# Kernel tuning notes

Measured on AMD Instinct MI355X. Metric: run time of the kernel, lower is better.

The kernel has to match this reference:

```python
import jax, jax.numpy as jnp
import numpy as np

NUM_HEADS = 32
NUM_KV_HEADS = 8
HEAD_DIM = 128
ROPE_THETA = 10000.0


def _rope_cos_sin(seq_len, head_dim, dtype):
    inv_freq = 1.0 / (ROPE_THETA ** (jnp.arange(0, head_dim, 2, dtype=jnp.float32) / head_dim))
    t = jnp.arange(seq_len, dtype=jnp.float32)
    freqs = jnp.outer(t, inv_freq)              # [S, hd/2]
    emb = jnp.concatenate([freqs, freqs], axis=-1)  # [S, hd]
    return jnp.cos(emb).astype(dtype), jnp.sin(emb).astype(dtype)


def _rotate_half(x):
    h = x.shape[-1] // 2
    return jnp.concatenate([-x[..., h:], x[..., :h]], axis=-1)


def _apply_rope(x, cos, sin):
    # x: [B, H, S, D]; cos/sin: [S, D] (position_ids = arange(S) in prefill)
    return x * cos[None, None] + _rotate_half(x) * sin[None, None]


def setup_inputs() -> dict:
    key = jax.random.key(0)
    ks = jax.random.split(key, 5)
    B, S, H = 1, 2048, 4096
    return {
        "hidden_states": jax.random.normal(ks[0], (B, S, H), dtype=jnp.float32),
        "Wq": jax.random.normal(ks[1], (H, NUM_HEADS * HEAD_DIM), dtype=jnp.float32) * 0.02,
        "Wk": jax.random.normal(ks[2], (H, NUM_KV_HEADS * HEAD_DIM), dtype=jnp.float32) * 0.02,
        "Wv": jax.random.normal(ks[3], (H, NUM_KV_HEADS * HEAD_DIM), dtype=jnp.float32) * 0.02,
        "Wo": jax.random.normal(ks[4], (NUM_HEADS * HEAD_DIM, H), dtype=jnp.float32) * 0.02,
    }


def reference(hidden_states, Wq, Wk, Wv, Wo):
    B, S, H = hidden_states.shape
    nh, nkv, hd = NUM_HEADS, NUM_KV_HEADS, HEAD_DIM
    groups = nh // nkv

    # fused QKV projections (bias-free, Llama-style)
    q = (hidden_states @ Wq).reshape(B, S, nh, hd).transpose(0, 2, 1, 3)   # [B,nh,S,D]
    k = (hidden_states @ Wk).reshape(B, S, nkv, hd).transpose(0, 2, 1, 3)  # [B,nkv,S,D]
    v = (hidden_states @ Wv).reshape(B, S, nkv, hd).transpose(0, 2, 1, 3)

    # inline RoPE on q and k
    cos, sin = _rope_cos_sin(S, hd, q.dtype)
    q = _apply_rope(q, cos, sin)
    k = _apply_rope(k, cos, sin)

    # GQA: repeat kv heads to match query heads (num_key_value_groups)
    k = jnp.repeat(k, groups, axis=1)  # [B,nh,S,D]
    v = jnp.repeat(v, groups, axis=1)

    scale = 1.0 / jnp.sqrt(jnp.asarray(hd, dtype=q.dtype))
    logits = jnp.einsum("bhqd,bhkd->bhqk", q, k) * scale  # [B,nh,S,S]

    # prefill causal mask (phys_past_len = 0)
    causal = jnp.tril(jnp.ones((S, S), dtype=bool))
    neg = jnp.asarray(jnp.finfo(logits.dtype).min, dtype=logits.dtype)
    logits = jnp.where(causal[None, None], logits, neg)

    attn = jax.nn.softmax(logits.astype(jnp.float32), axis=-1).astype(q.dtype)
    out = jnp.einsum("bhqk,bhkd->bhqd", attn, v)           # [B,nh,S,D]
    out = out.transpose(0, 2, 1, 3).reshape(B, S, nh * hd)  # [B,S,H]
    return out @ Wo
```

## Files before the change

### kernel.cpp

```cpp
#include <hip/hip_runtime.h>
#include <cstdint>
#include <cstddef>

typedef __attribute__((ext_vector_type(4))) float f32x4;
typedef __attribute__((ext_vector_type(16))) float f32x16;
typedef __attribute__((ext_vector_type(8))) short bf16x8;
typedef __attribute__((ext_vector_type(2))) unsigned int u32x2;

#define S_LEN   2048
#define HID     4096
#define NH      32
#define NKV     8
#define HD      128
#define QKV_N   6144

typedef const __attribute__((address_space(1))) unsigned int* gptr_t;
typedef __attribute__((address_space(3))) unsigned int* lptr_t;

__device__ __forceinline__ void gload_lds16(const void* g, void* l) {
  __builtin_amdgcn_global_load_lds((gptr_t)g, (lptr_t)l, 16, 0, 0);
}

__device__ __forceinline__ ushort f2bf(float f) {
  union { float f; uint32_t u; } v; v.f = f;
  uint32_t r = v.u + 0x7FFFu + ((v.u >> 16) & 1u);
  return (ushort)(r >> 16);
}
__device__ __forceinline__ float bf2f(ushort u) {
  union { uint32_t u; float f; } v; v.u = ((uint32_t)u) << 16;
  return v.f;
}

__global__ void cast_f32_bf16(const float* __restrict__ in, ushort* __restrict__ out, int n) {
  int i = (blockIdx.x * 256 + threadIdx.x) * 4;
  if (i >= n) return;
  float4 v = *reinterpret_cast<const float4*>(in + i);
  ushort4 o;
  o.x = f2bf(v.x); o.y = f2bf(v.y); o.z = f2bf(v.z); o.w = f2bf(v.w);
  *reinterpret_cast<ushort4*>(out + i) = o;
}

__global__ void transpose_cast(const float* __restrict__ in, ushort* __restrict__ out, int R, int C) {
  __shared__ float t[32][33];
  int tx = threadIdx.x & 31, ty = threadIdx.x >> 5;
  int r0 = blockIdx.y * 32, c0 = blockIdx.x * 32;
#pragma unroll
  for (int i = 0; i < 32; i += 8)
    t[ty + i][tx] = in[(size_t)(r0 + ty + i) * C + c0 + tx];
  __syncthreads();
#pragma unroll
  for (int i = 0; i < 32; i += 8)
    out[(size_t)(c0 + ty + i) * R + r0 + tx] = f2bf(t[tx][ty + i]);
}

template <bool BF16_OUT>
__global__ __launch_bounds__(256, 4) void gemm_bt(
    const ushort* __restrict__ A, const ushort* __restrict__ B,
    void* __restrict__ Cp, int M, int N, int K) {
  __shared__ ushort a_lds[128 * 32];
  __shared__ ushort b_lds[128 * 32];
  const int tid = threadIdx.x;
  const int wid = tid >> 6, lane = tid & 63;
  const int l16 = lane & 15, lk = lane >> 4;
  const int wr = wid >> 1, wc = wid & 1;
  const size_t a_row0 = (size_t)blockIdx.y * 128;
  const size_t b_row0 = (size_t)blockIdx.x * 128;

  f32x4 acc[4][4] = {};
  const int pswz = lk ^ (l16 & 3) ^ ((l16 >> 2) & 1);

  for (int kt = 0; kt < K; kt += 32) {
    __syncthreads();
#pragma unroll
    for (int i = 0; i < 2; ++i) {
      int c = i * 256 + tid;
      int row = c >> 2, p = c & 3;
      int gch = p ^ (row & 3) ^ ((row >> 2) & 1);
      gload_lds16(A + (a_row0 + row) * K + kt + gch * 8, &a_lds[c * 8]);
      gload_lds16(B + (b_row0 + row) * K + kt + gch * 8, &b_lds[c * 8]);
    }
    __syncthreads();

    bf16x8 af[4], bf[4];
#pragma unroll
    for (int m = 0; m < 4; ++m) {
      int row = wr * 64 + m * 16 + l16;
      af[m] = *reinterpret_cast<const bf16x8*>(&a_lds[row * 32 + pswz * 8]);
    }
#pragma unroll
    for (int n = 0; n < 4; ++n) {
      int row = wc * 64 + n * 16 + l16;
      bf[n] = *reinterpret_cast<const bf16x8*>(&b_lds[row * 32 + pswz * 8]);
    }
#pragma unroll
    for (int m = 0; m < 4; ++m)
#pragma unroll
      for (int n = 0; n < 4; ++n)
        acc[m][n] = __builtin_amdgcn_mfma_f32_16x16x32_bf16(af[m], bf[n], acc[m][n], 0, 0, 0);
  }

#pragma unroll
  for (int m = 0; m < 4; ++m) {
    int row_b = wr * 64 + m * 16 + lk * 4;
#pragma unroll
    for (int n = 0; n < 4; ++n) {
      int col = (int)b_row0 + wc * 64 + n * 16 + l16;
#pragma unroll
      for (int r = 0; r < 4; ++r) {
        size_t row = a_row0 + row_b + r;
        if constexpr (BF16_OUT)
          ((ushort*)Cp)[row * N + col] = f2bf(acc[m][n][r]);
        else
          ((float*)Cp)[row * N + col] = acc[m][n][r];
      }
    }
  }
}

__global__ void rope_kernel(ushort* __restrict__ QKV) {
  int idx = blockIdx.x * 256 + threadIdx.x;
  int dg = idx & 7;
  int t = idx >> 3;
  int s = t / 40;
  int hh = t - s * 40;
  if (s >= S_LEN) return;
  int col = (hh < NH) ? hh * HD : HID + (hh - NH) * HD;
  ushort* base = QKV + (size_t)s * QKV_N + col + dg * 8;

  union U { uint4 v; ushort u[8]; };
  U L, H, OL, OH;
  L.v = *reinterpret_cast<const uint4*>(base);
  H.v = *reinterpret_cast<const uint4*>(base + 64);
  const float C0 = 13.287712379549449f / 64.0f;
#pragma unroll
  for (int j = 0; j < 8; ++j) {
    int d = dg * 8 + j;
    float invf = exp2f(-(float)d * C0);
    float ang = (float)s * invf;
    float sn, cs;
    sincosf(ang, &sn, &cs);
    float xl = bf2f(L.u[j]), xh = bf2f(H.u[j]);
    OL.u[j] = f2bf(xl * cs - xh * sn);
    OH.u[j] = f2bf(xh * cs + xl * sn);
  }
  *reinterpret_cast<uint4*>(base) = OL.v;
  *reinterpret_cast<uint4*>(base + 64) = OH.v;
}

__global__ void transpose_v(const ushort* __restrict__ QKV, ushort* __restrict__ Vt) {
  __shared__ ushort t[64][65];
  int s0 = blockIdx.x * 64;
  int d0 = blockIdx.y * 64;
  int hkv = blockIdx.z;
  int tx = threadIdx.x & 63, ty = threadIdx.x >> 6;
#pragma unroll
  for (int i = 0; i < 64; i += 4)
    t[i + ty][tx] = QKV[(size_t)(s0 + i + ty) * QKV_N + HID + NKV * HD + hkv * HD + d0 + tx];
  __syncthreads();
#pragma unroll
  for (int i = 0; i < 64; i += 4)
    Vt[((size_t)hkv * HD + d0 + i + ty) * S_LEN + s0 + tx] = t[tx][i + ty];
}

__global__ __launch_bounds__(256, 2) void attn_kernel(
    const ushort* __restrict__ QKV, const ushort* __restrict__ Vt, ushort* __restrict__ AO) {
  constexpr float SCALE = 0.08838834764831845f;
  __shared__ ushort k_lds[2][64 * 128];
  __shared__ ushort v_lds[2][128 * 64];

  const int lin = blockIdx.x;
  const int h = ((lin & 7) << 2) + ((lin >> 3) & 3);
  const int p = lin >> 5;
  const int hkv = h >> 2;
  const int tid = threadIdx.x, wid = tid >> 6, lane = tid & 63;
  const int l32 = lane & 31;
  const int hi = lane >> 5;

  auto stageKV = [&](int buf, int kt) {
#pragma unroll
    for (int i = 0; i < 4; ++i) {
      int c = i * 256 + wid * 64 + lane;
      int row = c >> 4, ch = c & 15;
      int sch = ch ^ (row & 7);
      gload_lds16(QKV + (size_t)(kt * 64 + row) * QKV_N + HID + hkv * HD + sch * 8,
                  &k_lds[buf][c * 8]);
    }
#pragma unroll
    for (int i = 0; i < 4; ++i) {
      int c = i * 256 + wid * 64 + lane;
      int row = c >> 3, ch = c & 7;
      int sch = ch ^ (row & 7);
      gload_lds16(Vt + ((size_t)hkv * HD + row) * S_LEN + (size_t)kt * 64 + sch * 8,
                  &v_lds[buf][c * 8]);
    }
  };

  for (int pi = 0; pi < 2; ++pi) {
    const int qb = pi ? (15 - p) : p;
    const int q0 = qb * 128;
    const int qg = q0 + wid * 32 + l32;

    bf16x8 qf[8];
    {
      const ushort* qrow = QKV + (size_t)qg * QKV_N + h * HD + hi * 8;
#pragma unroll
      for (int ds = 0; ds < 8; ++ds)
        qf[ds] = *reinterpret_cast<const bf16x8*>(qrow + ds * 16);
    }

    float m_run = -1e30f, l_run = 0.f;
    f32x16 oacc[4] = {};

    stageKV(0, 0);
    __syncthreads();

    const int nt = 2 * qb + 2;
    for (int kt = 0; kt < nt; ++kt) {
      const int cur = kt & 1;
      if (kt + 1 < nt) stageKV(cur ^ 1, kt + 1);

      if (kt * 64 <= q0 + wid * 32 + 31) {
        float pv[32];
        __builtin_amdgcn_s_setprio(1);
#pragma unroll
        for (int kf = 0; kf < 2; ++kf) {
          f32x16 s = {};
          int rk = kf * 32 + l32;
#pragma unroll
          for (int ds = 0; ds < 8; ++ds) {
            int c16 = (ds * 2 + hi) ^ (rk & 7);
            bf16x8 kfr = *reinterpret_cast<const bf16x8*>(&k_lds[cur][rk * 128 + c16 * 8]);
            s = __builtin_amdgcn_mfma_f32_32x32x16_bf16(kfr, qf[ds], s, 0, 0, 0);
          }
#pragma unroll
          for (int r = 0; r < 16; ++r) pv[kf * 16 + r] = s[r] * SCALE;
        }
        __builtin_amdgcn_s_setprio(0);

        if (kt * 64 + 63 > q0 + wid * 32) {
#pragma unroll
          for (int kf = 0; kf < 2; ++kf)
#pragma unroll
            for (int r = 0; r < 16; ++r) {
              int kl = kf * 32 + (r & 3) + 8 * (r >> 2) + 4 * hi;
              if (kt * 64 + kl > qg) pv[kf * 16 + r] = -1e30f;
            }
        }

        float mt = pv[0];
#pragma unroll
        for (int i = 1; i < 32; ++i) mt = fmaxf(mt, pv[i]);
        mt = fmaxf(mt, __shfl_xor(mt, 32, 64));
        float mn = fmaxf(m_run, mt);
        float alpha = __expf(m_run - mn);
        float ls = 0.f;
#pragma unroll
        for (int i = 0; i < 32; ++i) { pv[i] = __expf(pv[i] - mn); ls += pv[i]; }
        ls += __shfl_xor(ls, 32, 64);
        l_run = l_run * alpha + ls;
        m_run = mn;
#pragma unroll
        for (int f = 0; f < 4; ++f)
#pragma unroll
          for (int r = 0; r < 16; ++r) oacc[f][r] *= alpha;

        union PW { uint32_t w[4]; bf16x8 v; } pa[4];
#pragma unroll
        for (int ks = 0; ks < 4; ++ks) {
          uint32_t x0, x1, y0, y1;
          asm("v_cvt_pk_bf16_f32 %0, %1, %2" : "=v"(x0) : "v"(pv[8 * ks + 0]), "v"(pv[8 * ks + 1]));
          asm("v_cvt_pk_bf16_f32 %0, %1, %2" : "=v"(x1) : "v"(pv[8 * ks + 2]), "v"(pv[8 * ks + 3]));
          asm("v_cvt_pk_bf16_f32 %0, %1, %2" : "=v"(y0) : "v"(pv[8 * ks + 4]), "v"(pv[8 * ks + 5]));
          asm("v_cvt_pk_bf16_f32 %0, %1, %2" : "=v"(y1) : "v"(pv[8 * ks + 6]), "v"(pv[8 * ks + 7]));
          u32x2 r0 = __builtin_amdgcn_permlane32_swap(x0, y0, false, false);
          u32x2 r1 = __builtin_amdgcn_permlane32_swap(x1, y1, false, false);
          pa[ks].w[0] = r0.x; pa[ks].w[1] = r1.x; pa[ks].w[2] = r0.y; pa[ks].w[3] = r1.y;
        }

        __builtin_amdgcn_s_setprio(1);
#pragma unroll
        for (int ks = 0; ks < 4; ++ks) {
#pragma unroll
          for (int f = 0; f < 4; ++f) {
            int dv = f * 32 + l32;
            int c8 = (2 * ks + hi) ^ (dv & 7);
            bf16x8 vfr = *reinterpret_cast<const bf16x8*>(&v_lds[cur][dv * 64 + c8 * 8]);
            oacc[f] = __builtin_amdgcn_mfma_f32_32x32x16_bf16(vfr, pa[ks].v, oacc[f], 0, 0, 0);
          }
        }
        __builtin_amdgcn_s_setprio(0);
      }

      __syncthreads();
    }

    float inv_l = 1.0f / l_run;
    ushort* aorow = AO + (size_t)qg * HID + h * HD;
#pragma unroll
    for (int f = 0; f < 4; ++f)
#pragma unroll
      for (int g = 0; g < 4; ++g) {
        ushort4 o;
        o.x = f2bf(oacc[f][g * 4 + 0] * inv_l);
        o.y = f2bf(oacc[f][g * 4 + 1] * inv_l);
        o.z = f2bf(oacc[f][g * 4 + 2] * inv_l);
        o.w = f2bf(oacc[f][g * 4 + 3] * inv_l);
        *reinterpret_cast<ushort4*>(aorow + f * 32 + g * 8 + 4 * hi) = o;
      }
  }
}

extern "C" void kernel_launch(void* const* d_in, const int* in_sizes, int n_in,
                              void* d_out, int out_size, void* d_ws, size_t ws_size,
                              hipStream_t stream) {
  (void)in_sizes; (void)n_in; (void)out_size;
  const float* hs = (const float*)d_in[0];
  const float* Wq = (const float*)d_in[1];
  const float* Wk = (const float*)d_in[2];
  const float* Wv = (const float*)d_in[3];
  const float* Wo = (const float*)d_in[4];
  float* out = (float*)d_out;

  char* ws = (char*)d_ws;
  const size_t OFF_HSB   = 0;
  const size_t OFF_WQKVT = OFF_HSB + 16777216;
  const size_t OFF_WOT   = OFF_WQKVT + 50331648;
  const size_t OFF_QKV   = OFF_WOT + 33554432;
  const size_t OFF_VT    = OFF_QKV + 25165824;
  const size_t OFF_AO    = OFF_VT + 4194304;
  if (ws_size < OFF_AO + 16777216) return;

  ushort* hsb   = (ushort*)(ws + OFF_HSB);
  ushort* WqkvT = (ushort*)(ws + OFF_WQKVT);
  ushort* WoT   = (ushort*)(ws + OFF_WOT);
  ushort* QKV   = (ushort*)(ws + OFF_QKV);
  ushort* Vt    = (ushort*)(ws + OFF_VT);
  ushort* AO    = (ushort*)(ws + OFF_AO);

  cast_f32_bf16<<<8192, 256, 0, stream>>>(hs, hsb, S_LEN * HID);
  transpose_cast<<<dim3(4096 / 32, 4096 / 32), 256, 0, stream>>>(Wq, WqkvT, HID, 4096);
  transpose_cast<<<dim3(1024 / 32, 4096 / 32), 256, 0, stream>>>(Wk, WqkvT + (size_t)4096 * HID, HID, 1024);
  transpose_cast<<<dim3(1024 / 32, 4096 / 32), 256, 0, stream>>>(Wv, WqkvT + (size_t)5120 * HID, HID, 1024);
  transpose_cast<<<dim3(4096 / 32, 4096 / 32), 256, 0, stream>>>(Wo, WoT, 4096, HID);

  gemm_bt<true><<<dim3(QKV_N / 128, S_LEN / 128), 256, 0, stream>>>(hsb, WqkvT, QKV, S_LEN, QKV_N, HID);
  rope_kernel<<<(S_LEN * 40 * 8) / 256, 256, 0, stream>>>(QKV);
  transpose_v<<<dim3(S_LEN / 64, HD / 64, NKV), 256, 0, stream>>>(QKV, Vt);
  attn_kernel<<<256, 256, 0, stream>>>(QKV, Vt, AO);
  gemm_bt<false><<<dim3(HID / 128, S_LEN / 128), 256, 0, stream>>>(AO, WoT, out, S_LEN, HID, HID);
}
```

Before: 355.1 us.

## Replace GEMM with triple-buffered pipelined 128x256 tile kernel using 8 waves

Swaps the single-buffered 128x128 GEMM for a 512-thread kernel with 128x256 tiles and a three-slot LDS ring. Global-to-LDS loads for k-tile t+2 are issued while computing tile t, synchronised with explicit vmcnt waits and raw barriers. The B fragment reads are split into two halves interleaved with MFMA bursts under raised wave priority, and the LDS swizzle pattern changes. The aim is to hide global load latency and raise MFMA utilisation in the QKV and output projections, at the cost of more LDS per block and fragile hand-tuned waitcnt counts.

```diff
diff --git a/kernel.cpp b/kernel.cpp
--- a/kernel.cpp
+++ b/kernel.cpp
@@ -53,65 +53,114 @@
     out[(size_t)(c0 + ty + i) * R + r0 + tx] = f2bf(t[tx][ty + i]);
 }
 
-template <bool BF16_OUT>
-__global__ __launch_bounds__(256, 4) void gemm_bt(
+template <int BM, bool BF16_OUT>
+__global__ __launch_bounds__(512, 2) void gemm_pipe(
     const ushort* __restrict__ A, const ushort* __restrict__ B,
-    void* __restrict__ Cp, int M, int N, int K) {
-  __shared__ ushort a_lds[128 * 32];
-  __shared__ ushort b_lds[128 * 32];
+    void* __restrict__ Cp, int N, int K) {
+  constexpr int MR = BM / 32;
+  constexpr int ALOADS = BM / 128;
+  __shared__ ushort a_lds[3][BM * 32];
+  __shared__ ushort b_lds[3][256 * 32];
   const int tid = threadIdx.x;
   const int wid = tid >> 6, lane = tid & 63;
   const int l16 = lane & 15, lk = lane >> 4;
-  const int wr = wid >> 1, wc = wid & 1;
-  const size_t a_row0 = (size_t)blockIdx.y * 128;
-  const size_t b_row0 = (size_t)blockIdx.x * 128;
-
-  f32x4 acc[4][4] = {};
-  const int pswz = lk ^ (l16 & 3) ^ ((l16 >> 2) & 1);
-
-  for (int kt = 0; kt < K; kt += 32) {
-    __syncthreads();
+  const int wr = wid >> 2, wc = wid & 3;
+  const size_t a_row0 = (size_t)blockIdx.y * BM;
+  const size_t b_row0 = (size_t)blockIdx.x * 256;
+
+  f32x4 acc[MR][4] = {};
+  const int NT = K >> 5;
+  const int cswz = lk ^ ((l16 >> 1) & 3);
+
+  auto stageA = [&](int slot, int t) {
+    const size_t kb = (size_t)t << 5;
+#pragma unroll
+    for (int i = 0; i < ALOADS; ++i) {
+      int c = i * 512 + tid;
+      int row = c >> 2, p = c & 3;
+      int src = p ^ ((row >> 1) & 3);
+      gload_lds16(A + (a_row0 + row) * K + kb + src * 8, &a_lds[slot][c * 8]);
+    }
+  };
+  auto stageB = [&](int slot, int t) {
+    const size_t kb = (size_t)t << 5;
 #pragma unroll
     for (int i = 0; i < 2; ++i) {
-      int c = i * 256 + tid;
+      int c = i * 512 + tid;
       int row = c >> 2, p = c & 3;
-      int gch = p ^ (row & 3) ^ ((row >> 2) & 1);
-      gload_lds16(A + (a_row0 + row) * K + kt + gch * 8, &a_lds[c * 8]);
-      gload_lds16(B + (b_row0 + row) * K + kt + gch * 8, &b_lds[c * 8]);
-    }
-    __syncthreads();
-
-    bf16x8 af[4], bf[4];
-#pragma unroll
-    for (int m = 0; m < 4; ++m) {
-      int row = wr * 64 + m * 16 + l16;
-      af[m] = *reinterpret_cast<const bf16x8*>(&a_lds[row * 32 + pswz * 8]);
-    }
-#pragma unroll
-    for (int n = 0; n < 4; ++n) {
+      int src = p ^ ((row >> 1) & 3);
+      gload_lds16(B + (b_row0 + row) * K + kb + src * 8, &b_lds[slot][c * 8]);
+    }
+  };
+
+  stageA(0, 0); stageB(0, 0);
+  stageA(1, 1); stageB(1, 1);
+
+  for (int t = 0; t < NT; ++t) {
+    const int cur = t % 3;
+
+    if (t + 2 < NT) stageA((t + 2) % 3, t + 2);
+    if (t < NT - 2) {
+      if constexpr (BM == 256) asm volatile("s_waitcnt vmcnt(6)" ::: "memory");
+      else                     asm volatile("s_waitcnt vmcnt(4)" ::: "memory");
+    } else if (t == NT - 2) {
+      if constexpr (BM == 256) asm volatile("s_waitcnt vmcnt(4)" ::: "memory");
+      else                     asm volatile("s_waitcnt vmcnt(3)" ::: "memory");
+    } else {
+      asm volatile("s_waitcnt vmcnt(0)" ::: "memory");
+    }
+    __builtin_amdgcn_s_barrier();
+
+    bf16x8 af[MR], b01[2], b23[2];
+#pragma unroll
+    for (int m = 0; m < MR; ++m) {
+      int row = wr * (BM / 2) + m * 16 + l16;
+      af[m] = *reinterpret_cast<const bf16x8*>(&a_lds[cur][row * 32 + cswz * 8]);
+    }
+#pragma unroll
+    for (int n = 0; n < 2; ++n) {
       int row = wc * 64 + n * 16 + l16;
-      bf[n] = *reinterpret_cast<const bf16x8*>(&b_lds[row * 32 + pswz * 8]);
-    }
-#pragma unroll
-    for (int m = 0; m < 4; ++m)
-#pragma unroll
-      for (int n = 0; n < 4; ++n)
-        acc[m][n] = __builtin_amdgcn_mfma_f32_16x16x32_bf16(af[m], bf[n], acc[m][n], 0, 0, 0);
+      b01[n] = *reinterpret_cast<const bf16x8*>(&b_lds[cur][row * 32 + cswz * 8]);
+    }
+    asm volatile("s_waitcnt lgkmcnt(0)" ::: "memory");
+    __builtin_amdgcn_s_setprio(1);
+#pragma unroll
+    for (int m = 0; m < MR; ++m)
+#pragma unroll
+      for (int n = 0; n < 2; ++n)
+        acc[m][n] = __builtin_amdgcn_mfma_f32_16x16x32_bf16(af[m], b01[n], acc[m][n], 0, 0, 0);
+    __builtin_amdgcn_s_setprio(0);
+    __builtin_amdgcn_s_barrier();
+
+    if (t + 2 < NT) stageB((t + 2) % 3, t + 2);
+#pragma unroll
+    for (int n = 0; n < 2; ++n) {
+      int row = wc * 64 + 32 + n * 16 + l16;
+      b23[n] = *reinterpret_cast<const bf16x8*>(&b_lds[cur][row * 32 + cswz * 8]);
+    }
+    asm volatile("s_waitcnt lgkmcnt(0)" ::: "memory");
+    __builtin_amdgcn_s_setprio(1);
+#pragma unroll
+    for (int m = 0; m < MR; ++m)
+#pragma unroll
+      for (int n = 0; n < 2; ++n)
+        acc[m][2 + n] = __builtin_amdgcn_mfma_f32_16x16x32_bf16(af[m], b23[n], acc[m][2 + n], 0, 0, 0);
+    __builtin_amdgcn_s_setprio(0);
+    __builtin_amdgcn_s_barrier();
   }
 
 #pragma unroll
-  for (int m = 0; m < 4; ++m) {
-    int row_b = wr * 64 + m * 16 + lk * 4;
+  for (int m = 0; m < MR; ++m) {
+    size_t row_b = a_row0 + wr * (BM / 2) + m * 16 + lk * 4;
 #pragma unroll
     for (int n = 0; n < 4; ++n) {
       int col = (int)b_row0 + wc * 64 + n * 16 + l16;
 #pragma unroll
       for (int r = 0; r < 4; ++r) {
-        size_t row = a_row0 + row_b + r;
         if constexpr (BF16_OUT)
-          ((ushort*)Cp)[row * N + col] = f2bf(acc[m][n][r]);
+          ((ushort*)Cp)[(row_b + r) * N + col] = f2bf(acc[m][n][r]);
         else
-          ((float*)Cp)[row * N + col] = acc[m][n][r];
+          ((float*)Cp)[(row_b + r) * N + col] = acc[m][n][r];
       }
     }
   }
@@ -343,9 +392,9 @@
   transpose_cast<<<dim3(1024 / 32, 4096 / 32), 256, 0, stream>>>(Wv, WqkvT + (size_t)5120 * HID, HID, 1024);
   transpose_cast<<<dim3(4096 / 32, 4096 / 32), 256, 0, stream>>>(Wo, WoT, 4096, HID);
 
-  gemm_bt<true><<<dim3(QKV_N / 128, S_LEN / 128), 256, 0, stream>>>(hsb, WqkvT, QKV, S_LEN, QKV_N, HID);
+  gemm_pipe<128, true><<<dim3(QKV_N / 256, S_LEN / 128), 512, 0, stream>>>(hsb, WqkvT, QKV, QKV_N, HID);
   rope_kernel<<<(S_LEN * 40 * 8) / 256, 256, 0, stream>>>(QKV);
   transpose_v<<<dim3(S_LEN / 64, HD / 64, NKV), 256, 0, stream>>>(QKV, Vt);
   attn_kernel<<<256, 256, 0, stream>>>(QKV, Vt, AO);
-  gemm_bt<false><<<dim3(HID / 128, S_LEN / 128), 256, 0, stream>>>(AO, WoT, out, S_LEN, HID, HID);
-}
+  gemm_pipe<128, false><<<dim3(HID / 256, S_LEN / 128), 512, 0, stream>>>(AO, WoT, out, HID, HID);
+}
```

After: 422.4 us. +19.0%, slower.

## Co-schedule paired query blocks in 512-thread attention and split-K the output projection

Applied to the files above, without the earlier changes.

The attention kernel now runs 8 waves per block. The two paired causal query blocks are processed at the same time instead of one after the other, so each staged K/V tile is shared by both halves and the per-block work is balanced. The output projection is split along K into two half-depth GEMMs that write fp32 partials into reused workspace, followed by an elementwise add kernel. This raises block count and occupancy for the final GEMM, at the cost of extra fp32 partial traffic and one more launch. The attention loop also stages two K/V tiles past the end of the sequence that are never used.

```diff
diff --git a/kernel.cpp b/kernel.cpp
--- a/kernel.cpp
+++ b/kernel.cpp
@@ -117,6 +117,79 @@
   }
 }
 
+__global__ __launch_bounds__(256, 4) void gemm_o_ks(
+    const ushort* __restrict__ A, const ushort* __restrict__ B,
+    float* __restrict__ P0, float* __restrict__ P1) {
+  __shared__ ushort a_lds[128 * 32];
+  __shared__ ushort b_lds[128 * 32];
+  const int bid = blockIdx.x;
+  const int kh = bid >> 9;
+  const int rem = bid & 511;
+  const size_t b_row0 = (size_t)(rem & 31) * 128;
+  const size_t a_row0 = (size_t)(rem >> 5) * 128;
+  const int k0 = kh * 2048, k1 = k0 + 2048;
+  float* __restrict__ P = kh ? P1 : P0;
+  const int tid = threadIdx.x;
+  const int wid = tid >> 6, lane = tid & 63;
+  const int l16 = lane & 15, lk = lane >> 4;
+  const int wr = wid >> 1, wc = wid & 1;
+
+  f32x4 acc[4][4] = {};
+  const int pswz = lk ^ (l16 & 3) ^ ((l16 >> 2) & 1);
+
+  for (int kt = k0; kt < k1; kt += 32) {
+    __syncthreads();
+#pragma unroll
+    for (int i = 0; i < 2; ++i) {
+      int c = i * 256 + tid;
+      int row = c >> 2, p = c & 3;
+      int gch = p ^ (row & 3) ^ ((row >> 2) & 1);
+      gload_lds16(A + (a_row0 + row) * HID + kt + gch * 8, &a_lds[c * 8]);
+      gload_lds16(B + (b_row0 + row) * HID + kt + gch * 8, &b_lds[c * 8]);
+    }
+    __syncthreads();
+
+    bf16x8 af[4], bf[4];
+#pragma unroll
+    for (int m = 0; m < 4; ++m) {
+      int row = wr * 64 + m * 16 + l16;
+      af[m] = *reinterpret_cast<const bf16x8*>(&a_lds[row * 32 + pswz * 8]);
+    }
+#pragma unroll
+    for (int n = 0; n < 4; ++n) {
+      int row = wc * 64 + n * 16 + l16;
+      bf[n] = *reinterpret_cast<const bf16x8*>(&b_lds[row * 32 + pswz * 8]);
+    }
+#pragma unroll
+    for (int m = 0; m < 4; ++m)
+#pragma unroll
+      for (int n = 0; n < 4; ++n)
+        acc[m][n] = __builtin_amdgcn_mfma_f32_16x16x32_bf16(af[m], bf[n], acc[m][n], 0, 0, 0);
+  }
+
+#pragma unroll
+  for (int m = 0; m < 4; ++m) {
+    int row_b = wr * 64 + m * 16 + lk * 4;
+#pragma unroll
+    for (int n = 0; n < 4; ++n) {
+      int col = (int)b_row0 + wc * 64 + n * 16 + l16;
+#pragma unroll
+      for (int r = 0; r < 4; ++r)
+        P[(a_row0 + row_b + r) * HID + col] = acc[m][n][r];
+    }
+  }
+}
+
+__global__ void add_f32(const float* __restrict__ a, const float* __restrict__ b,
+                        float* __restrict__ o, int n) {
+  int i = (blockIdx.x * 256 + threadIdx.x) * 4;
+  if (i >= n) return;
+  float4 x = *reinterpret_cast<const float4*>(a + i);
+  float4 y = *reinterpret_cast<const float4*>(b + i);
+  float4 z; z.x = x.x + y.x; z.y = x.y + y.y; z.z = x.z + y.z; z.w = x.w + y.w;
+  *reinterpret_cast<float4*>(o + i) = z;
+}
+
 __global__ void rope_kernel(ushort* __restrict__ QKV) {
   int idx = blockIdx.x * 256 + threadIdx.x;
   int dg = idx & 7;
@@ -162,7 +235,7 @@
     Vt[((size_t)hkv * HD + d0 + i + ty) * S_LEN + s0 + tx] = t[tx][i + ty];
 }
 
-__global__ __launch_bounds__(256, 2) void attn_kernel(
+__global__ __launch_bounds__(512, 2) void attn_kernel(
     const ushort* __restrict__ QKV, const ushort* __restrict__ Vt, ushort* __restrict__ AO) {
   constexpr float SCALE = 0.08838834764831845f;
   __shared__ ushort k_lds[2][64 * 128];
@@ -170,24 +243,38 @@
 
   const int lin = blockIdx.x;
   const int h = ((lin & 7) << 2) + ((lin >> 3) & 3);
-  const int p = lin >> 5;
+  const int pr = lin >> 5;
   const int hkv = h >> 2;
-  const int tid = threadIdx.x, wid = tid >> 6, lane = tid & 63;
+  const int tid = threadIdx.x, w = tid >> 6, lane = tid & 63;
   const int l32 = lane & 31;
   const int hi = lane >> 5;
+  const int qb = (w < 4) ? (15 - pr) : pr;
+  const int q0w = qb * 128 + (w & 3) * 32;
+  const int qg = q0w + l32;
+
+  bf16x8 qf[8];
+  {
+    const ushort* qrow = QKV + (size_t)qg * QKV_N + h * HD + hi * 8;
+#pragma unroll
+    for (int ds = 0; ds < 8; ++ds)
+      qf[ds] = *reinterpret_cast<const bf16x8*>(qrow + ds * 16);
+  }
+
+  float m_run = -1e30f, l_run = 0.f;
+  f32x16 oacc[4] = {};
 
   auto stageKV = [&](int buf, int kt) {
 #pragma unroll
-    for (int i = 0; i < 4; ++i) {
-      int c = i * 256 + wid * 64 + lane;
+    for (int i = 0; i < 2; ++i) {
+      int c = i * 512 + tid;
       int row = c >> 4, ch = c & 15;
       int sch = ch ^ (row & 7);
       gload_lds16(QKV + (size_t)(kt * 64 + row) * QKV_N + HID + hkv * HD + sch * 8,
                   &k_lds[buf][c * 8]);
     }
 #pragma unroll
-    for (int i = 0; i < 4; ++i) {
-      int c = i * 256 + wid * 64 + lane;
+    for (int i = 0; i < 2; ++i) {
+      int c = i * 512 + tid;
       int row = c >> 3, ch = c & 7;
       int sch = ch ^ (row & 7);
       gload_lds16(Vt + ((size_t)hkv * HD + row) * S_LEN + (size_t)kt * 64 + sch * 8,
@@ -195,119 +282,102 @@
     }
   };
 
-  for (int pi = 0; pi < 2; ++pi) {
-    const int qb = pi ? (15 - p) : p;
-    const int q0 = qb * 128;
-    const int qg = q0 + wid * 32 + l32;
-
-    bf16x8 qf[8];
-    {
-      const ushort* qrow = QKV + (size_t)qg * QKV_N + h * HD + hi * 8;
-#pragma unroll
-      for (int ds = 0; ds < 8; ++ds)
-        qf[ds] = *reinterpret_cast<const bf16x8*>(qrow + ds * 16);
-    }
-
-    float m_run = -1e30f, l_run = 0.f;
-    f32x16 oacc[4] = {};
-
-    stageKV(0, 0);
+  const int NT = 34 - 2 * pr;
+  stageKV(0, 0);
+  __syncthreads();
+
+  for (int kt = 0; kt < NT; ++kt) {
+    const int cur = kt & 1;
+    if (kt + 1 < NT) stageKV(cur ^ 1, kt + 1);
+
+    if (kt * 64 <= q0w + 31) {
+      float pv[32];
+      __builtin_amdgcn_s_setprio(1);
+#pragma unroll
+      for (int kf = 0; kf < 2; ++kf) {
+        f32x16 s = {};
+        int rk = kf * 32 + l32;
+#pragma unroll
+        for (int ds = 0; ds < 8; ++ds) {
+          int c16 = (ds * 2 + hi) ^ (rk & 7);
+          bf16x8 kfr = *reinterpret_cast<const bf16x8*>(&k_lds[cur][rk * 128 + c16 * 8]);
+          s = __builtin_amdgcn_mfma_f32_32x32x16_bf16(kfr, qf[ds], s, 0, 0, 0);
+        }
+#pragma unroll
+        for (int r = 0; r < 16; ++r) pv[kf * 16 + r] = s[r] * SCALE;
+      }
+      __builtin_amdgcn_s_setprio(0);
+
+      if (kt * 64 + 63 > q0w) {
+#pragma unroll
+        for (int kf = 0; kf < 2; ++kf)
+#pragma unroll
+          for (int r = 0; r < 16; ++r) {
+            int kl = kf * 32 + (r & 3) + 8 * (r >> 2) + 4 * hi;
+            if (kt * 64 + kl > qg) pv[kf * 16 + r] = -1e30f;
+          }
+      }
+
+      float mt = pv[0];
+#pragma unroll
+      for (int i = 1; i < 32; ++i) mt = fmaxf(mt, pv[i]);
+      mt = fmaxf(mt, __shfl_xor(mt, 32, 64));
+      float mn = fmaxf(m_run, mt);
+      float alpha = __expf(m_run - mn);
+      float ls = 0.f;
+#pragma unroll
+      for (int i = 0; i < 32; ++i) { pv[i] = __expf(pv[i] - mn); ls += pv[i]; }
+      ls += __shfl_xor(ls, 32, 64);
+      l_run = l_run * alpha + ls;
+      m_run = mn;
+#pragma unroll
+      for (int f = 0; f < 4; ++f)
+#pragma unroll
+        for (int r = 0; r < 16; ++r) oacc[f][r] *= alpha;
+
+      union PW { uint32_t w[4]; bf16x8 v; } pa[4];
+#pragma unroll
+      for (int ks = 0; ks < 4; ++ks) {
+        uint32_t x0, x1, y0, y1;
+        asm("v_cvt_pk_bf16_f32 %0, %1, %2" : "=v"(x0) : "v"(pv[8 * ks + 0]), "v"(pv[8 * ks + 1]));
+        asm("v_cvt_pk_bf16_f32 %0, %1, %2" : "=v"(x1) : "v"(pv[8 * ks + 2]), "v"(pv[8 * ks + 3]));
+        asm("v_cvt_pk_bf16_f32 %0, %1, %2" : "=v"(y0) : "v"(pv[8 * ks + 4]), "v"(pv[8 * ks + 5]));
+        asm("v_cvt_pk_bf16_f32 %0, %1, %2" : "=v"(y1) : "v"(pv[8 * ks + 6]), "v"(pv[8 * ks + 7]));
+        u32x2 r0 = __builtin_amdgcn_permlane32_swap(x0, y0, false, false);
+        u32x2 r1 = __builtin_amdgcn_permlane32_swap(x1, y1, false, false);
+        pa[ks].w[0] = r0.x; pa[ks].w[1] = r1.x; pa[ks].w[2] = r0.y; pa[ks].w[3] = r1.y;
+      }
+
+      __builtin_amdgcn_s_setprio(1);
+#pragma unroll
+      for (int ks = 0; ks < 4; ++ks) {
+#pragma unroll
+        for (int f = 0; f < 4; ++f) {
+          int dv = f * 32 + l32;
+          int c8 = (2 * ks + hi) ^ (dv & 7);
+          bf16x8 vfr = *reinterpret_cast<const bf16x8*>(&v_lds[cur][dv * 64 + c8 * 8]);
+          oacc[f] = __builtin_amdgcn_mfma_f32_32x32x16_bf16(vfr, pa[ks].v, oacc[f], 0, 0, 0);
+        }
+      }
+      __builtin_amdgcn_s_setprio(0);
+    }
+
     __syncthreads();
-
-    const int nt = 2 * qb + 2;
-    for (int kt = 0; kt < nt; ++kt) {
-      const int cur = kt & 1;
-      if (kt + 1 < nt) stageKV(cur ^ 1, kt + 1);
-
-      if (kt * 64 <= q0 + wid * 32 + 31) {
-        float pv[32];
-        __builtin_amdgcn_s_setprio(1);
-#pragma unroll
-        for (int kf = 0; kf < 2; ++kf) {
-          f32x16 s = {};
-          int rk = kf * 32 + l32;
-#pragma unroll
-          for (int ds = 0; ds < 8; ++ds) {
-            int c16 = (ds * 2 + hi) ^ (rk & 7);
-            bf16x8 kfr = *reinterpret_cast<const bf16x8*>(&k_lds[cur][rk * 128 + c16 * 8]);
-            s = __builtin_amdgcn_mfma_f32_32x32x16_bf16(kfr, qf[ds], s, 0, 0, 0);
-          }
-#pragma unroll
-          for (int r = 0; r < 16; ++r) pv[kf * 16 + r] = s[r] * SCALE;
-        }
-        __builtin_amdgcn_s_setprio(0);
-
-        if (kt * 64 + 63 > q0 + wid * 32) {
-#pragma unroll
-          for (int kf = 0; kf < 2; ++kf)
-#pragma unroll
-            for (int r = 0; r < 16; ++r) {
-              int kl = kf * 32 + (r & 3) + 8 * (r >> 2) + 4 * hi;
-              if (kt * 64 + kl > qg) pv[kf * 16 + r] = -1e30f;
-            }
-        }
-
-        float mt = pv[0];
-#pragma unroll
-        for (int i = 1; i < 32; ++i) mt = fmaxf(mt, pv[i]);
-        mt = fmaxf(mt, __shfl_xor(mt, 32, 64));
-        float mn = fmaxf(m_run, mt);
-        float alpha = __expf(m_run - mn);
-        float ls = 0.f;
-#pragma unroll
-        for (int i = 0; i < 32; ++i) { pv[i] = __expf(pv[i] - mn); ls += pv[i]; }
-        ls += __shfl_xor(ls, 32, 64);
-        l_run = l_run * alpha + ls;
-        m_run = mn;
-#pragma unroll
-        for (int f = 0; f < 4; ++f)
-#pragma unroll
-          for (int r = 0; r < 16; ++r) oacc[f][r] *= alpha;
-
-        union PW { uint32_t w[4]; bf16x8 v; } pa[4];
-#pragma unroll
-        for (int ks = 0; ks < 4; ++ks) {
-          uint32_t x0, x1, y0, y1;
-          asm("v_cvt_pk_bf16_f32 %0, %1, %2" : "=v"(x0) : "v"(pv[8 * ks + 0]), "v"(pv[8 * ks + 1]));
-          asm("v_cvt_pk_bf16_f32 %0, %1, %2" : "=v"(x1) : "v"(pv[8 * ks + 2]), "v"(pv[8 * ks + 3]));
-          asm("v_cvt_pk_bf16_f32 %0, %1, %2" : "=v"(y0) : "v"(pv[8 * ks + 4]), "v"(pv[8 * ks + 5]));
-          asm("v_cvt_pk_bf16_f32 %0, %1, %2" : "=v"(y1) : "v"(pv[8 * ks + 6]), "v"(pv[8 * ks + 7]));
-          u32x2 r0 = __builtin_amdgcn_permlane32_swap(x0, y0, false, false);
-          u32x2 r1 = __builtin_amdgcn_permlane32_swap(x1, y1, false, false);
-          pa[ks].w[0] = r0.x; pa[ks].w[1] = r1.x; pa[ks].w[2] = r0.y; pa[ks].w[3] = r1.y;
-        }
-
-        __builtin_amdgcn_s_setprio(1);
-#pragma unroll
-        for (int ks = 0; ks < 4; ++ks) {
-#pragma unroll
-          for (int f = 0; f < 4; ++f) {
-            int dv = f * 32 + l32;
-            int c8 = (2 * ks + hi) ^ (dv & 7);
-            bf16x8 vfr = *reinterpret_cast<const bf16x8*>(&v_lds[cur][dv * 64 + c8 * 8]);
-            oacc[f] = __builtin_amdgcn_mfma_f32_32x32x16_bf16(vfr, pa[ks].v, oacc[f], 0, 0, 0);
-          }
-        }
-        __builtin_amdgcn_s_setprio(0);
-      }
-
-      __syncthreads();
-    }
-
-    float inv_l = 1.0f / l_run;
-    ushort* aorow = AO + (size_t)qg * HID + h * HD;
-#pragma unroll
-    for (int f = 0; f < 4; ++f)
-#pragma unroll
-      for (int g = 0; g < 4; ++g) {
-        ushort4 o;
-        o.x = f2bf(oacc[f][g * 4 + 0] * inv_l);
-        o.y = f2bf(oacc[f][g * 4 + 1] * inv_l);
-        o.z = f2bf(oacc[f][g * 4 + 2] * inv_l);
-        o.w = f2bf(oacc[f][g * 4 + 3] * inv_l);
-        *reinterpret_cast<ushort4*>(aorow + f * 32 + g * 8 + 4 * hi) = o;
-      }
-  }
+  }
+
+  float inv_l = 1.0f / l_run;
+  ushort* aorow = AO + (size_t)qg * HID + h * HD;
+#pragma unroll
+  for (int f = 0; f < 4; ++f)
+#pragma unroll
+    for (int g = 0; g < 4; ++g) {
+      ushort4 o;
+      o.x = f2bf(oacc[f][g * 4 + 0] * inv_l);
+      o.y = f2bf(oacc[f][g * 4 + 1] * inv_l);
+      o.z = f2bf(oacc[f][g * 4 + 2] * inv_l);
+      o.w = f2bf(oacc[f][g * 4 + 3] * inv_l);
+      *reinterpret_cast<ushort4*>(aorow + f * 32 + g * 8 + 4 * hi) = o;
+    }
 }
 
 extern "C" void kernel_launch(void* const* d_in, const int* in_sizes, int n_in,
@@ -336,6 +406,8 @@
   ushort* QKV   = (ushort*)(ws + OFF_QKV);
   ushort* Vt    = (ushort*)(ws + OFF_VT);
   ushort* AO    = (ushort*)(ws + OFF_AO);
+  float* P0 = (float*)(ws + 0);
+  float* P1 = (float*)(ws + 33554432);
 
   cast_f32_bf16<<<8192, 256, 0, stream>>>(hs, hsb, S_LEN * HID);
   transpose_cast<<<dim3(4096 / 32, 4096 / 32), 256, 0, stream>>>(Wq, WqkvT, HID, 4096);
@@ -346,6 +418,7 @@
   gemm_bt<true><<<dim3(QKV_N / 128, S_LEN / 128), 256, 0, stream>>>(hsb, WqkvT, QKV, S_LEN, QKV_N, HID);
   rope_kernel<<<(S_LEN * 40 * 8) / 256, 256, 0, stream>>>(QKV);
   transpose_v<<<dim3(S_LEN / 64, HD / 64, NKV), 256, 0, stream>>>(QKV, Vt);
-  attn_kernel<<<256, 256, 0, stream>>>(QKV, Vt, AO);
-  gemm_bt<false><<<dim3(HID / 128, S_LEN / 128), 256, 0, stream>>>(AO, WoT, out, S_LEN, HID, HID);
-}
+  attn_kernel<<<256, 512, 0, stream>>>(QKV, Vt, AO);
+  gemm_o_ks<<<1024, 256, 0, stream>>>(AO, WoT, P0, P1);
+  add_f32<<<8192, 256, 0, stream>>>(P0, P1, out, S_LEN * HID);
+}
```

Result: no change. 362.0 us (+2.0%).
